# Kernel optimization log

Hardware: AMD Instinct MI355X
Metric: run time of the kernel (lower is better)

The kernel has to match this reference:

```python
import jax, jax.numpy as jnp
from jax import lax
import numpy as np

BATCH, SEQ_LEN, ENC_IN, C_OUT = 16, 512, 32, 32
N_ORDER = 256           # window_size
MULTISCALE = (1, 2, 4)
MODES = min(32, SEQ_LEN // 2)  # = 32


def make_hippo(N, dt):
    """HiPPO-LegT transition, bilinear (Tustin) discretization, Legendre eval matrix."""
    Q = np.arange(N, dtype=np.float64)
    R = (2 * Q + 1)[:, None]
    j, i = np.meshgrid(Q, Q)
    A = np.where(i < j, -1.0, (-1.0) ** (i - j + 1)) * R
    B = (-1.0) ** Q[:, None] * R                      # [N,1]
    I = np.eye(N)
    M = I - (dt / 2.0) * A
    Ad = np.linalg.solve(M, I + (dt / 2.0) * A)
    Bd = np.linalg.solve(M, dt * B).squeeze(-1)       # [N]
    vals = np.arange(0.0, 1.0, dt)
    x = 1.0 - 2.0 * vals
    P = np.zeros((N, len(vals)))
    P[0] = 1.0
    if N > 1:
        P[1] = x
    for n in range(1, N - 1):
        P[n + 1] = ((2 * n + 1) * x * P[n] - n * P[n - 1]) / (n + 1)
    E = P.T                                           # [len(vals), N]
    return Ad.astype(np.float32), Bd.astype(np.float32), E.astype(np.float32)


def setup_inputs():
    key = jax.random.key(0)
    ks = jax.random.split(key, 12)
    inp = {}
    inp['x_enc'] = jax.random.normal(ks[0], (BATCH, SEQ_LEN, ENC_IN), jnp.float32)
    inp['x_mark_enc'] = jax.random.normal(ks[1], (BATCH, SEQ_LEN, 4), jnp.float32)
    inp['x_dec'] = jax.random.normal(ks[2], (BATCH, SEQ_LEN, ENC_IN), jnp.float32)
    inp['x_mark_dec'] = jax.random.normal(ks[3], (BATCH, SEQ_LEN, 4), jnp.float32)
    inp['affine_weight'] = jnp.ones((1, 1, ENC_IN), jnp.float32)
    inp['affine_bias'] = jnp.zeros((1, 1, ENC_IN), jnp.float32)
    scale = 1.0 / (N_ORDER * N_ORDER)
    for s in range(3):
        inp[f'wr{s}'] = scale * jax.random.uniform(ks[4 + 2 * s], (N_ORDER, N_ORDER, MODES), jnp.float32)
        inp[f'wi{s}'] = scale * jax.random.uniform(ks[5 + 2 * s], (N_ORDER, N_ORDER, MODES), jnp.float32)
    inp['mlp_w'] = 0.1 * jax.random.normal(ks[10], (1, 3), jnp.float32)
    inp['mlp_b'] = jnp.zeros((1,), jnp.float32)
    inp['proj_w'] = 0.02 * jax.random.normal(ks[11], (ENC_IN, C_OUT), jnp.float32)
    inp['proj_b'] = jnp.zeros((C_OUT,), jnp.float32)
    for s, m in enumerate(MULTISCALE):
        A, Bv, E = make_hippo(N_ORDER, 1.0 / SEQ_LEN / m)
        inp[f'A{s}'] = jnp.asarray(A)
        inp[f'Bv{s}'] = jnp.asarray(Bv)
        inp[f'E{s}'] = jnp.asarray(E)
    return inp


def _hippo_scan(x, A, Bv):
    # x: [B, L, C] -> cs: [L, B, C, N]; c_t = A c_{t-1} + B f_t (applied on last dim)
    B_, L, C = x.shape
    c0 = jnp.zeros((B_, C, A.shape[0]), x.dtype)
    At = A.T
    def step(c, f):                      # f: [B, C]
        c = c @ At + f[..., None] * Bv
        return c, c
    _, cs = lax.scan(step, c0, jnp.transpose(x, (1, 0, 2)))
    return cs


def _spectral_conv(xc, wr, wi):
    # xc: [B, C, N, L]; keep first MODES rfft bins, complex channel mix over N, irfft
    L = xc.shape[-1]
    xf = jnp.fft.rfft(xc)                                # [B,C,N,L//2+1] complex64
    W = (wr + 1j * wi).astype(jnp.complex64)             # [N,N,MODES]
    out = jnp.einsum('bjix,iox->bjox', xf[..., :MODES], W)
    out_ft = jnp.pad(out, ((0, 0), (0, 0), (0, 0), (0, L // 2 + 1 - MODES)))
    return jnp.fft.irfft(out_ft, n=L)                    # [B,C,N,L]


def _forward(x_enc, affine_weight, affine_bias, specs, mlp_w, mlp_b, proj_w, proj_b, hippos):
    means = lax.stop_gradient(jnp.mean(x_enc, axis=1, keepdims=True))
    xc = x_enc - means
    stdev = lax.stop_gradient(jnp.sqrt(jnp.var(xc, axis=1, keepdims=True) + 1e-5))
    x = xc / stdev
    x = x * affine_weight + affine_bias                  # [B, L, C]
    pred_len = SEQ_LEN
    decs = []
    for (wr, wi), (A, Bv, E) in zip(specs, hippos):
        # multiscale slice x[:, -m*pred_len:] clips to full seq_len since pred_len==seq_len
        cs = _hippo_scan(x, A, Bv)                       # [L,B,C,N]
        x_in_c = jnp.transpose(cs, (1, 2, 3, 0))         # [B,C,N,L]
        out1 = _spectral_conv(x_in_c, wr, wi)            # [B,C,N,L]
        x_dec_c = out1[..., pred_len - 1]                # [B,C,N]
        dec = x_dec_c @ E[-pred_len:, :].T               # [B,C,pred_len]
        decs.append(dec)
    stacked = jnp.stack(decs, axis=-1)                   # [B,C,P,3]
    y = stacked @ mlp_w[0] + mlp_b[0]                    # Linear(3,1) + squeeze -> [B,C,P]
    y = jnp.transpose(y, (0, 2, 1))                      # [B,P,C]
    y = (y - affine_bias) / (affine_weight + 1e-10)
    y = y * stdev + means
    return y @ proj_w + proj_b                           # OutputBlock: per-step channel projection


def reference(x_enc, x_mark_enc, x_dec, x_mark_dec, affine_weight, affine_bias,
              wr0, wi0, wr1, wi1, wr2, wi2, mlp_w, mlp_b, proj_w, proj_b,
              A0, Bv0, E0, A1, Bv1, E1, A2, Bv2, E2):
    specs = [(wr0, wi0), (wr1, wi1), (wr2, wi2)]
    hippos = [(A0, Bv0, E0), (A1, Bv1, E1), (A2, Bv2, E2)]
    return _forward(x_enc, affine_weight, affine_bias, specs, mlp_w, mlp_b, proj_w, proj_b, hippos)
```

## Files before the change

### kernel.cpp

```cpp
#include <hip/hip_runtime.h>
#include <math.h>

#define SEQ 512
#define NORD 256
#define MODES 32
#define KBIG (NORD*MODES*2)
#define PI_F 3.14159265358979323846f

typedef _Float16 half8 __attribute__((ext_vector_type(8)));
typedef float floatx4 __attribute__((ext_vector_type(4)));


struct GJob {
  const float* A; const float* B; float* C; const float* scale_ptr;
  int M, N, lda, k0, k1, atomic;
};
struct GJobs { GJob j[6]; };

__global__ __launch_bounds__(256) void gemm32_k(GJobs P) {
  GJob jb = P.j[blockIdx.z];
  int col0 = blockIdx.x * 32;
  int row0 = blockIdx.y * 32;
  if (row0 >= jb.M || col0 >= jb.N) return;
  __shared__ float As[64][34];
  __shared__ float Bs[64][36];
  int tid = threadIdx.x;
  int tx = tid & 15, ty = tid >> 4;
  const float* A = jb.A; const float* B = jb.B;
  int M = jb.M, N = jb.N, lda = jb.lda;
  int kcA = (tid & 15) * 4, rA = tid >> 4;
  int ccB = (tid & 7) * 4, kkB = tid >> 3;
  int gr0 = row0 + rA, gr1 = row0 + rA + 16;
  const float4 z4 = make_float4(0.f, 0.f, 0.f, 0.f);
  float4 a0, a1, b0, b1;
  {
    int kb = jb.k0;
    a0 = (gr0 < M) ? *(const float4*)&A[(size_t)gr0 * lda + kb + kcA] : z4;
    a1 = (gr1 < M) ? *(const float4*)&A[(size_t)gr1 * lda + kb + kcA] : z4;
    b0 = *(const float4*)&B[(size_t)(kb + kkB) * N + col0 + ccB];
    b1 = *(const float4*)&B[(size_t)(kb + kkB + 32) * N + col0 + ccB];
  }
  float acc00 = 0.f, acc01 = 0.f, acc10 = 0.f, acc11 = 0.f;
  for (int kb = jb.k0; kb < jb.k1; kb += 64) {
    As[kcA+0][rA] = a0.x; As[kcA+1][rA] = a0.y; As[kcA+2][rA] = a0.z; As[kcA+3][rA] = a0.w;
    As[kcA+0][rA+16] = a1.x; As[kcA+1][rA+16] = a1.y; As[kcA+2][rA+16] = a1.z; As[kcA+3][rA+16] = a1.w;
    *(float4*)&Bs[kkB][ccB] = b0;
    *(float4*)&Bs[kkB+32][ccB] = b1;
    __syncthreads();
    if (kb + 64 < jb.k1) {
      int kn = kb + 64;
      a0 = (gr0 < M) ? *(const float4*)&A[(size_t)gr0 * lda + kn + kcA] : z4;
      a1 = (gr1 < M) ? *(const float4*)&A[(size_t)gr1 * lda + kn + kcA] : z4;
      b0 = *(const float4*)&B[(size_t)(kn + kkB) * N + col0 + ccB];
      b1 = *(const float4*)&B[(size_t)(kn + kkB + 32) * N + col0 + ccB];
    }
    #pragma unroll
    for (int k = 0; k < 64; k++) {
      float2 av = *(float2*)&As[k][ty * 2];
      float2 bv = *(float2*)&Bs[k][tx * 2];
      acc00 += av.x * bv.x; acc01 += av.x * bv.y;
      acc10 += av.y * bv.x; acc11 += av.y * bv.y;
    }
    __syncthreads();
  }
  float sc = jb.scale_ptr ? *jb.scale_ptr : 1.f;
  int gr = row0 + ty * 2, gc = col0 + tx * 2;
  float v00 = acc00 * sc, v01 = acc01 * sc, v10 = acc10 * sc, v11 = acc11 * sc;
  if (jb.atomic) {
    if (gr < M)     { atomicAdd(&jb.C[(size_t)gr * N + gc], v00);     atomicAdd(&jb.C[(size_t)gr * N + gc + 1], v01); }
    if (gr + 1 < M) { atomicAdd(&jb.C[(size_t)(gr+1) * N + gc], v10); atomicAdd(&jb.C[(size_t)(gr+1) * N + gc + 1], v11); }
  } else {
    if (gr < M)     { jb.C[(size_t)gr * N + gc] = v00;     jb.C[(size_t)gr * N + gc + 1] = v01; }
    if (gr + 1 < M) { jb.C[(size_t)(gr+1) * N + gc] = v10; jb.C[(size_t)(gr+1) * N + gc + 1] = v11; }
  }
}


__global__ __launch_bounds__(256) void prep2_k(const float* __restrict__ x_enc,
                                               const float* __restrict__ aw,
                                               const float* __restrict__ ab,
                                               float* __restrict__ F,
                                               float* __restrict__ stats,
                                               const float* A0, const float* A1, const float* A2,
                                               const float* B0, const float* B1, const float* B2,
                                               const float* E0, const float* E1, const float* E2,
                                               float* R, float* Kry, float* Et, float* Z) {
  __shared__ float tile[32][33];
  __shared__ float ws1[4], ws2[4];
  __shared__ float mean_s, istd_s;
  int bid = blockIdx.x;
  int tid = threadIdx.x;
  if (bid < 512) {
    int row = bid;
    int b = row >> 5, c = row & 31;
    const float* xp = x_enc + (size_t)b * SEQ * 32 + c;
    float v0 = xp[(size_t)tid * 32];
    float v1 = xp[(size_t)(tid + 256) * 32];
    float s = v0 + v1, s2 = v0 * v0 + v1 * v1;
    for (int off = 32; off; off >>= 1) {
      s  += __shfl_down(s,  off, 64);
      s2 += __shfl_down(s2, off, 64);
    }
    int wid = tid >> 6, lane = tid & 63;
    if (lane == 0) { ws1[wid] = s; ws2[wid] = s2; }
    __syncthreads();
    if (tid == 0) {
      float t1 = ws1[0] + ws1[1] + ws1[2] + ws1[3];
      float t2 = ws2[0] + ws2[1] + ws2[2] + ws2[3];
      float mean = t1 / 512.f;
      float var = t2 / 512.f - mean * mean;
      float sd = sqrtf(var + 1e-5f);
      mean_s = mean; istd_s = 1.f / sd;
      stats[row] = mean; stats[512 + row] = sd;
    }
    __syncthreads();
    float w = aw[c], bb = ab[c];
    float m = mean_s, is = istd_s;
    F[(size_t)row * SEQ + tid]       = (v0 - m) * is * w + bb;
    F[(size_t)row * SEQ + tid + 256] = (v1 - m) * is * w + bb;
  } else if (bid < 704) {
    int b2 = bid - 512;
    int scl = b2 >> 6, t = b2 & 63;
    int ti = t >> 3, tm = t & 7;
    const float* A = scl == 0 ? A0 : (scl == 1 ? A1 : A2);
    float* Rd = R + (size_t)scl * 2 * 65536;
    int tx = tid & 31, ty0 = tid >> 5;
    int i0 = ti * 32, m0 = tm * 32;
    #pragma unroll
    for (int r = 0; r < 4; r++) {
      int ty = ty0 + r * 8;
      tile[ty][tx] = A[(size_t)(i0 + ty) * 256 + m0 + tx];
    }
    __syncthreads();
    #pragma unroll
    for (int r = 0; r < 4; r++) {
      int ty = ty0 + r * 8;
      Rd[(size_t)(m0 + ty) * 256 + i0 + tx] = tile[tx][ty];
    }
  } else if (bid < 1088) {
    int b2 = bid - 704;
    int scl = b2 >> 7, t = b2 & 127;
    int tp = t >> 3, to = t & 7;
    const float* E; int rows;
    if (scl == 0) { E = E0; rows = 512; }
    else if (scl == 1) { E = E1; rows = 1024; }
    else { E = E2; rows = 2048; }
    int base = rows - 512;
    int p0 = tp * 32, o0 = to * 32;
    int tx = tid & 31, ty0 = tid >> 5;
    #pragma unroll
    for (int r = 0; r < 4; r++) {
      int ty = ty0 + r * 8;
      tile[ty][tx] = E[(size_t)(base + p0 + ty) * 256 + o0 + tx];
    }
    __syncthreads();
    #pragma unroll
    for (int r = 0; r < 4; r++) {
      int ty = ty0 + r * 8;
      Et[(size_t)scl * 131072 + (size_t)(o0 + ty) * 512 + p0 + tx] = tile[tx][ty];
    }
  } else if (bid < 1091) {
    int scl = bid - 1088;
    const float* B = scl == 0 ? B0 : (scl == 1 ? B1 : B2);
    Kry[(size_t)scl * 512 * 256 + tid] = B[tid];
  } else {
    int idx = (bid - 1091) * 256 + tid;
    ((float4*)Z)[idx] = make_float4(0.f, 0.f, 0.f, 0.f);
  }
}


__global__ __launch_bounds__(256) void qbuildB_k(const float* __restrict__ Kry,
                                                 const float2* __restrict__ Pp,
                                                 _Float16* __restrict__ Qf, int s0) {
  int bg = blockIdx.x;
  int slab = bg >> 8;
  int s = s0 + slab;
  int r = bg & 255;
  int ig = r & 31, c = r >> 5;
  const float* Kry_s = Kry + (size_t)s * 131072;
  const float2* P = Pp + (size_t)s * 65536;
  uint4* Qd4 = (uint4*)(Qf + (size_t)slab * 8388608);
  int tid = threadIdx.x;
  int k = tid & 31, il = tid >> 5;
  int i = ig * 8 + il;
  __shared__ __align__(16) unsigned int buf[16 * 260];
  float ar = 0.f, ai = 0.f;
  for (int cp = 0; cp < c; cp++) {
    float2 p = P[(size_t)(cp * 32 + k) * 256 + i];
    ar += p.x; ai += p.y;
  }
  const float step = 2.f * PI_F / 512.f;
  int m0 = c * 64;
  int st_low = tid & 15;
  int part_base = tid >> 4;
  for (int mb = 0; mb < 64; mb += 16) {
    #pragma unroll
    for (int mm = 0; mm < 16; mm++) {
      int m = m0 + mb + mm;
      float kap = Kry_s[(size_t)m * 256 + i];
      float sn, cn; __sincosf(step * (float)((k * m) & 511), &sn, &cn);
      ar += kap * cn; ai -= kap * sn;
      int st = 511 - m;
      float sn2, cn2; __sincosf(step * (float)((k * st) & 511), &sn2, &cn2);
      float qr = ar * cn2 + ai * sn2;
      float qi = ai * cn2 - ar * sn2;
      qr = fminf(fmaxf(qr, -60000.f), 60000.f);
      qi = fminf(fmaxf(qi, -60000.f), 60000.f);
      _Float16 h0 = (_Float16)qr, h1 = (_Float16)qi;
      unsigned short u0, u1;
      __builtin_memcpy(&u0, &h0, 2); __builtin_memcpy(&u1, &h1, 2);
      buf[(st & 15) * 260 + il * 32 + k] = (unsigned int)u0 | ((unsigned int)u1 << 16);
    }
    __syncthreads();
    int st_base = 496 - m0 - mb;
    int st = st_base + st_low;
    size_t rowbase = (size_t)(st >> 4) * 512;
    #pragma unroll
    for (int p = 0; p < 4; p++) {
      int part = part_base + p * 16;
      int ilw = part >> 3, k4 = part & 7;
      int iw = ig * 8 + ilw;
      size_t g = (rowbase + (size_t)(iw * 2 + (k4 >> 2))) * 64
               + (size_t)((k4 & 3) * 16 + st_low);
      Qd4[g] = *(const uint4*)&buf[st_low * 260 + ilw * 32 + k4 * 4];
    }
    __syncthreads();
  }
}


__global__ __launch_bounds__(256) void qw_k(const float* __restrict__ Kry,
                                            float2* __restrict__ Pp,
                                            const float* wr0, const float* wi0,
                                            const float* wr1, const float* wi1,
                                            const float* wr2, const float* wi2,
                                            _Float16* __restrict__ Wt, int s0, int nA) {
  int bid = blockIdx.x;
  int tid = threadIdx.x;
  if (bid < nA) {
    int bg = bid;
    int s = s0 + (bg >> 8);
    int r = bg & 255;
    int k = r & 31, c = r >> 5;
    const float* Kry_s = Kry + (size_t)s * 131072;
    float2* P = Pp + (size_t)s * 65536;
    int i = tid;
    float ar = 0.f, ai = 0.f;
    const float step = 2.f * PI_F / 512.f;
    int m0 = c * 64;
    for (int mm = 0; mm < 64; mm++) {
      int m = m0 + mm;
      float kap = Kry_s[(size_t)m * 256 + i];
      float sn, cn; __sincosf(step * (float)((k * m) & 511), &sn, &cn);
      ar += kap * cn; ai -= kap * sn;
    }
    P[(size_t)(c * 32 + k) * 256 + i] = make_float2(ar, ai);
  } else {
    int bg = bid - nA;
    int slab = bg >> 8;
    int s = s0 + slab;
    int r = bg & 255;
    int og = r >> 3, iq = r & 7;
    const float* wr = s == 0 ? wr0 : (s == 1 ? wr1 : wr2);
    const float* wi = s == 0 ? wi0 : (s == 1 ? wi1 : wi2);
    unsigned int* Wd = (unsigned int*)(Wt + (size_t)slab * 4194304);
    int ol = tid >> 5, k = tid & 31;
    int o = og * 8 + ol;
    float sn, cn; __sincosf((2.f * PI_F / 512.f) * (float)k, &sn, &cn);
    float g = ((k == 0) ? (1.f / 512.f) : (2.f / 512.f)) * 4096.f;
    float gc = g * cn, gs = g * sn;
    size_t obase = (size_t)(o >> 4) * 512;
    int osub = (((k >> 2) & 3) * 16 + (o & 15)) * 4 + (k & 3);
    for (int ii = 0; ii < 32; ii++) {
      int i = iq * 32 + ii;
      float a = wr[(size_t)i * 8192 + o * 32 + k];
      float b = wi[(size_t)i * 8192 + o * 32 + k];
      float v0 = gc * a + gs * b;
      float v1 = gs * a - gc * b;
      _Float16 h0 = (_Float16)v0, h1 = (_Float16)v1;
      unsigned short u0, u1;
      __builtin_memcpy(&u0, &h0, 2); __builtin_memcpy(&u1, &h1, 2);
      Wd[(obase + (size_t)(i * 2 + (k >> 4))) * 256 + osub] = (unsigned int)u0 | ((unsigned int)u1 << 16);
    }
  }
}


__global__ __launch_bounds__(256) void umfma_k(const _Float16* __restrict__ Qf,
                                               const _Float16* __restrict__ Wt,
                                               float* __restrict__ U, int s0) {
  __shared__ __align__(16) _Float16 lds[2][12288];
  int kslab = blockIdx.x;
  int y = blockIdx.y;
  int slab = blockIdx.z;
  int s = s0 + slab;
  int mtb = y >> 1, ntb = y & 1;
  const _Float16* Q = Qf + (size_t)slab * 8388608;
  const _Float16* W = Wt + (size_t)slab * 4194304;
  float* Us = U + (size_t)s * 131072;
  int tid = threadIdx.x;
  int w = tid >> 6, lane = tid & 63;
  int wm = w >> 1, wn = w & 1;
  int quad = lane >> 4, lm = lane & 15;
  int mt0g = mtb * 4;
  int nt0g = ntb * 8;
  int ktg0 = kslab * 32;
  size_t laneoff = (size_t)lane * 8;

  floatx4 acc[2][4];
  #pragma unroll
  for (int a = 0; a < 2; a++)
    #pragma unroll
    for (int b = 0; b < 4; b++) acc[a][b] = (floatx4)(0.f);

  auto stage = [&](int ks, int bufi) {
    int ktg = ktg0 + ks * 2;
    #pragma unroll
    for (int q = 0; q < 6; q++) {
      int f = w * 6 + q;
      const _Float16* src;
      if (f < 8) {
        src = Q + (((size_t)(mt0g + (f >> 1)) * 512) + (size_t)(ktg + (f & 1))) * 512;
      } else {
        int g = f - 8;
        src = W + (((size_t)(nt0g + (g >> 1)) * 512) + (size_t)(ktg + (g & 1))) * 512;
      }
      __builtin_amdgcn_global_load_lds(
          (const __attribute__((address_space(1))) unsigned int*)(src + laneoff),
          (__attribute__((address_space(3))) unsigned int*)&lds[bufi][f * 512],
          16, 0, 0);
    }
  };

  stage(0, 0);
  __syncthreads();
  int buf = 0;
  for (int ks = 0; ks < 16; ks++) {
    if (ks < 15) stage(ks + 1, buf ^ 1);
    half8 a[2][2], b[4][2];
    #pragma unroll
    for (int mi2 = 0; mi2 < 2; mi2++)
      #pragma unroll
      for (int kk = 0; kk < 2; kk++)
        a[mi2][kk] = *(const half8*)&lds[buf][(size_t)(((wm * 2 + mi2) * 2 + kk) * 512) + laneoff];
    #pragma unroll
    for (int ni2 = 0; ni2 < 4; ni2++)
      #pragma unroll
      for (int kk = 0; kk < 2; kk++)
        b[ni2][kk] = *(const half8*)&lds[buf][(size_t)(4096 + ((wn * 4 + ni2) * 2 + kk) * 512) + laneoff];
    #pragma unroll
    for (int kk = 0; kk < 2; kk++)
      #pragma unroll
      for (int mi2 = 0; mi2 < 2; mi2++)
        #pragma unroll
        for (int ni2 = 0; ni2 < 4; ni2++)
          acc[mi2][ni2] = __builtin_amdgcn_mfma_f32_16x16x32_f16(a[mi2][kk], b[ni2][kk], acc[mi2][ni2], 0, 0, 0);
    __syncthreads();
    buf ^= 1;
  }

  const float sc = 1.f / 4096.f;
  #pragma unroll
  for (int mi2 = 0; mi2 < 2; mi2++) {
    int R0 = (mt0g + wm * 2 + mi2) * 16 + quad * 4;
    #pragma unroll
    for (int ni2 = 0; ni2 < 4; ni2++) {
      int gc = (nt0g + wn * 4 + ni2) * 16 + lm;
      #pragma unroll
      for (int rr2 = 0; rr2 < 4; rr2++)
        atomicAdd(&Us[(size_t)(R0 + rr2) * 256 + gc], acc[mi2][ni2][rr2] * sc);
    }
  }
}


__global__ __launch_bounds__(256) void final_k(const float* __restrict__ y0,
                                               const float* __restrict__ stats,
                                               const float* __restrict__ aw,
                                               const float* __restrict__ ab,
                                               const float* __restrict__ mlp_b,
                                               const float* __restrict__ pw,
                                               const float* __restrict__ pb,
                                               float* __restrict__ out) {
  int b = blockIdx.y;
  int p0 = blockIdx.x * 8;
  int tid = threadIdx.x;
  __shared__ float ys[32 * 8];
  __shared__ float pws[32 * 32];
  for (int t = tid; t < 1024; t += 256) pws[t] = pw[t];
  int c = tid >> 3, pl = tid & 7;
  int row = b * 32 + c;
  float mean = stats[row], sd = stats[512 + row];
  float raw = y0[(size_t)row * 512 + p0 + pl];
  float v = ((raw + mlp_b[0]) - ab[c]) / (aw[c] + 1e-10f) * sd + mean;
  ys[c * 8 + pl] = v;
  __syncthreads();
  int co = tid & 31; int pl2 = tid >> 5;
  float accv = pb[co];
  #pragma unroll
  for (int cc = 0; cc < 32; cc++) accv += ys[cc * 8 + pl2] * pws[cc * 32 + co];
  out[(size_t)b * 512 * 32 + (size_t)(p0 + pl2) * 32 + co] = accv;
}


extern "C" void kernel_launch(void* const* d_in, const int* in_sizes, int n_in,
                              void* d_out, int out_size, void* d_ws, size_t ws_size,
                              hipStream_t stream) {
  const float* x_enc = (const float*)d_in[0];
  const float* aw = (const float*)d_in[4];
  const float* ab = (const float*)d_in[5];
  const float* wr[3] = {(const float*)d_in[6], (const float*)d_in[8], (const float*)d_in[10]};
  const float* wi[3] = {(const float*)d_in[7], (const float*)d_in[9], (const float*)d_in[11]};
  const float* mlp_w = (const float*)d_in[12];
  const float* mlp_b = (const float*)d_in[13];
  const float* proj_w = (const float*)d_in[14];
  const float* proj_b = (const float*)d_in[15];
  const float* Am[3]  = {(const float*)d_in[16], (const float*)d_in[19], (const float*)d_in[22]};
  const float* Bv[3]  = {(const float*)d_in[17], (const float*)d_in[20], (const float*)d_in[23]};
  const float* Em[3]  = {(const float*)d_in[18], (const float*)d_in[21], (const float*)d_in[24]};

  float* w = (float*)d_ws;
  float* F     = w; w += 512 * 512;
  float* stats = w; w += 1024;
  float* Kry   = w; w += 3 * 512 * 256;
  float* R     = w; w += 3 * 2 * 65536;
  float* U     = w; w += 3 * 512 * 256;
  float* Ttot  = w; w += 512 * 512;
  float* Et    = w; w += 3 * 256 * 512;
  float* y0    = w; w += 512 * 512;
  float* Pp    = w; w += 3 * 65536 * 2;
  _Float16* Qf = (_Float16*)w;

  size_t base_bytes = (size_t)((char*)Qf - (char*)d_ws);
  size_t slab_bytes = (size_t)(8388608 + 4194304) * 2;
  int nS = (ws_size >= base_bytes + 3 * slab_bytes) ? 3 : 1;
  _Float16* Wb = Qf + (size_t)nS * 8388608;

  prep2_k<<<1731, 256, 0, stream>>>(x_enc, aw, ab, F, stats,
                                    Am[0], Am[1], Am[2], Bv[0], Bv[1], Bv[2],
                                    Em[0], Em[1], Em[2], R, Kry, Et, U);

  for (int j = 0; j < 9; j++) {
    GJobs P{};
    int M = 1 << j;
    int cur = j & 1;
    int nz = 0;
    for (int s = 0; s < 3; s++) {
      float* Ks = Kry + (size_t)s * 131072;
      float* Rj = R + (size_t)s * 131072 + (size_t)cur * 65536;
      float* Rn = R + (size_t)s * 131072 + (size_t)(1 - cur) * 65536;
      P.j[nz++] = {Ks, Rj, Ks + (size_t)M * 256, nullptr, M, 256, 256, 0, 256, 0};
      if (j < 8) P.j[nz++] = {Rj, Rj, Rn, nullptr, 256, 256, 256, 0, 256, 0};
    }
    gemm32_k<<<dim3(8, 8, nz), 256, 0, stream>>>(P);
  }

  if (nS == 3) {
    qw_k<<<1536, 256, 0, stream>>>(Kry, (float2*)Pp, wr[0], wi[0], wr[1], wi[1],
                                   wr[2], wi[2], Wb, 0, 768);
    qbuildB_k<<<768, 256, 0, stream>>>(Kry, (const float2*)Pp, Qf, 0);
    umfma_k<<<dim3(16, 16, 3), 256, 0, stream>>>(Qf, Wb, U, 0);
  } else {
    for (int s = 0; s < 3; s++) {
      qw_k<<<512, 256, 0, stream>>>(Kry, (float2*)Pp, wr[0], wi[0], wr[1], wi[1],
                                    wr[2], wi[2], Wb, s, 256);
      qbuildB_k<<<256, 256, 0, stream>>>(Kry, (const float2*)Pp, Qf, s);
      umfma_k<<<dim3(16, 16, 1), 256, 0, stream>>>(Qf, Wb, U, s);
    }
  }

  {
    GJobs P{};
    for (int s = 0; s < 3; s++)
      P.j[s] = {U + (size_t)s * 131072, Et + (size_t)s * 131072, Ttot,
                mlp_w + s, 512, 512, 256, 0, 256, 1};
    gemm32_k<<<dim3(16, 16, 3), 256, 0, stream>>>(P);
  }

  {
    GJobs P{};
    P.j[0] = {F, Ttot, y0, nullptr, 512, 512, 512, 0, 512, 0};
    gemm32_k<<<dim3(16, 16, 1), 256, 0, stream>>>(P);
  }

  final_k<<<dim3(64, 16), 256, 0, stream>>>(y0, stats, aw, ab, mlp_b, proj_w, proj_b,
                                            (float*)d_out);
}
```

Before: 351.8 us.

## Fuse Krylov doubling GEMMs into cooperative kernel and move weight packing into prep

Replaces nine separate gemm32 launches for the Krylov power-doubling steps with one cooperative kernel that loops over steps, using grid-wide syncs between them and a register-prefetched tile loop. It also moves the fp16 spectral-weight packing out of qw_k into extra blocks of the prep kernel, so that work overlaps with the other prep tasks, and halves qw_k's grid. This is meant to cut launch overhead and idle gaps between the small dependent GEMMs. In exchange it relies on cooperative launch support and grid.sync cost, and falls back to the old launches if the cooperative launch fails.

```diff
diff --git a/kernel.cpp b/kernel.cpp
--- a/kernel.cpp
+++ b/kernel.cpp
@@ -1,5 +1,8 @@
 #include <hip/hip_runtime.h>
+#include <hip/hip_cooperative_groups.h>
 #include <math.h>
+
+namespace cg = cooperative_groups;
 
 #define SEQ 512
 #define NORD 256
@@ -76,6 +79,81 @@
 }
 
 
+__global__ __launch_bounds__(256) void kry_k(float* __restrict__ Kry,
+                                             float* __restrict__ R) {
+  cg::grid_group grid = cg::this_grid();
+  __shared__ float As[64][34];
+  __shared__ float Bs[64][36];
+  int tid = threadIdx.x;
+  int tx = tid & 15, ty = tid >> 4;
+  int kcA = (tid & 15) * 4, rA = tid >> 4;
+  int ccB = (tid & 7) * 4, kkB = tid >> 3;
+  const float4 z4 = make_float4(0.f, 0.f, 0.f, 0.f);
+  for (int j = 0; j < 9; j++) {
+    int M = 1 << j;
+    int mb = (M + 31) >> 5;
+    int tilesA = mb * 8;
+    int hasB = (j < 8) ? 64 : 0;
+    int tilesPer = tilesA + hasB;
+    int ntiles = tilesPer * 3;
+    int cur = j & 1;
+    for (int t = blockIdx.x; t < ntiles; t += gridDim.x) {
+      int s = t / tilesPer;
+      int r = t - s * tilesPer;
+      float* Ks = Kry + (size_t)s * 131072;
+      float* Rj = R + (size_t)s * 131072 + (size_t)cur * 65536;
+      float* Rn = R + (size_t)s * 131072 + (size_t)(1 - cur) * 65536;
+      const float* A; const float* B; float* C;
+      int Mj, row0, col0;
+      if (r < tilesA) {
+        A = Ks; B = Rj; C = Ks + (size_t)M * 256; Mj = M;
+        row0 = (r >> 3) * 32; col0 = (r & 7) * 32;
+      } else {
+        int r2 = r - tilesA;
+        A = Rj; B = Rj; C = Rn; Mj = 256;
+        row0 = (r2 >> 3) * 32; col0 = (r2 & 7) * 32;
+      }
+      int gr0 = row0 + rA, gr1 = row0 + rA + 16;
+      float4 a0, a1, b0, b1;
+      a0 = (gr0 < Mj) ? *(const float4*)&A[(size_t)gr0 * 256 + kcA] : z4;
+      a1 = (gr1 < Mj) ? *(const float4*)&A[(size_t)gr1 * 256 + kcA] : z4;
+      b0 = *(const float4*)&B[(size_t)kkB * 256 + col0 + ccB];
+      b1 = *(const float4*)&B[(size_t)(kkB + 32) * 256 + col0 + ccB];
+      float acc00 = 0.f, acc01 = 0.f, acc10 = 0.f, acc11 = 0.f;
+      for (int kb = 0; kb < 256; kb += 64) {
+        As[kcA+0][rA] = a0.x; As[kcA+1][rA] = a0.y; As[kcA+2][rA] = a0.z; As[kcA+3][rA] = a0.w;
+        As[kcA+0][rA+16] = a1.x; As[kcA+1][rA+16] = a1.y; As[kcA+2][rA+16] = a1.z; As[kcA+3][rA+16] = a1.w;
+        *(float4*)&Bs[kkB][ccB] = b0;
+        *(float4*)&Bs[kkB+32][ccB] = b1;
+        __syncthreads();
+        if (kb + 64 < 256) {
+          int kn = kb + 64;
+          a0 = (gr0 < Mj) ? *(const float4*)&A[(size_t)gr0 * 256 + kn + kcA] : z4;
+          a1 = (gr1 < Mj) ? *(const float4*)&A[(size_t)gr1 * 256 + kn + kcA] : z4;
+          b0 = *(const float4*)&B[(size_t)(kn + kkB) * 256 + col0 + ccB];
+          b1 = *(const float4*)&B[(size_t)(kn + kkB + 32) * 256 + col0 + ccB];
+        }
+        #pragma unroll
+        for (int k = 0; k < 64; k++) {
+          float2 av = *(float2*)&As[k][ty * 2];
+          float2 bv = *(float2*)&Bs[k][tx * 2];
+          acc00 += av.x * bv.x; acc01 += av.x * bv.y;
+          acc10 += av.y * bv.x; acc11 += av.y * bv.y;
+        }
+        __syncthreads();
+      }
+      int gr = row0 + ty * 2, gc = col0 + tx * 2;
+      if (gr < Mj)     { C[(size_t)gr * 256 + gc] = acc00;     C[(size_t)gr * 256 + gc + 1] = acc01; }
+      if (gr + 1 < Mj) { C[(size_t)(gr+1) * 256 + gc] = acc10; C[(size_t)(gr+1) * 256 + gc + 1] = acc11; }
+    }
+    if (j < 8) {
+      __threadfence();
+      grid.sync();
+    }
+  }
+}
+
+
 __global__ __launch_bounds__(256) void prep2_k(const float* __restrict__ x_enc,
                                                const float* __restrict__ aw,
                                                const float* __restrict__ ab,
@@ -84,7 +162,11 @@
                                                const float* A0, const float* A1, const float* A2,
                                                const float* B0, const float* B1, const float* B2,
                                                const float* E0, const float* E1, const float* E2,
-                                               float* R, float* Kry, float* Et, float* Z) {
+                                               float* R, float* Kry, float* Et, float* Z,
+                                               const float* wr0, const float* wi0,
+                                               const float* wr1, const float* wi1,
+                                               const float* wr2, const float* wi2,
+                                               _Float16* __restrict__ Wt) {
   __shared__ float tile[32][33];
   __shared__ float ws1[4], ws2[4];
   __shared__ float mean_s, istd_s;
@@ -163,9 +245,36 @@
     int scl = bid - 1088;
     const float* B = scl == 0 ? B0 : (scl == 1 ? B1 : B2);
     Kry[(size_t)scl * 512 * 256 + tid] = B[tid];
-  } else {
+  } else if (bid < 1731) {
     int idx = (bid - 1091) * 256 + tid;
     ((float4*)Z)[idx] = make_float4(0.f, 0.f, 0.f, 0.f);
+  } else {
+    int bg = bid - 1731;
+    int slab = bg >> 8;
+    int s = slab;
+    int r = bg & 255;
+    int og = r >> 3, iq = r & 7;
+    const float* wr = s == 0 ? wr0 : (s == 1 ? wr1 : wr2);
+    const float* wi = s == 0 ? wi0 : (s == 1 ? wi1 : wi2);
+    unsigned int* Wd = (unsigned int*)(Wt + (size_t)slab * 4194304);
+    int ol = tid >> 5, k = tid & 31;
+    int o = og * 8 + ol;
+    float sn, cn; __sincosf((2.f * PI_F / 512.f) * (float)k, &sn, &cn);
+    float g = ((k == 0) ? (1.f / 512.f) : (2.f / 512.f)) * 4096.f;
+    float gc = g * cn, gs = g * sn;
+    size_t obase = (size_t)(o >> 4) * 512;
+    int osub = (((k >> 2) & 3) * 16 + (o & 15)) * 4 + (k & 3);
+    for (int ii = 0; ii < 32; ii++) {
+      int i = iq * 32 + ii;
+      float a = wr[(size_t)i * 8192 + o * 32 + k];
+      float b = wi[(size_t)i * 8192 + o * 32 + k];
+      float v0 = gc * a + gs * b;
+      float v1 = gs * a - gc * b;
+      _Float16 h0 = (_Float16)v0, h1 = (_Float16)v1;
+      unsigned short u0, u1;
+      __builtin_memcpy(&u0, &h0, 2); __builtin_memcpy(&u1, &h1, 2);
+      Wd[(obase + (size_t)(i * 2 + (k >> 4))) * 256 + osub] = (unsigned int)u0 | ((unsigned int)u1 << 16);
+    }
   }
 }
 
@@ -437,28 +546,37 @@
   int nS = (ws_size >= base_bytes + 3 * slab_bytes) ? 3 : 1;
   _Float16* Wb = Qf + (size_t)nS * 8388608;
 
-  prep2_k<<<1731, 256, 0, stream>>>(x_enc, aw, ab, F, stats,
-                                    Am[0], Am[1], Am[2], Bv[0], Bv[1], Bv[2],
-                                    Em[0], Em[1], Em[2], R, Kry, Et, U);
-
-  for (int j = 0; j < 9; j++) {
-    GJobs P{};
-    int M = 1 << j;
-    int cur = j & 1;
-    int nz = 0;
-    for (int s = 0; s < 3; s++) {
-      float* Ks = Kry + (size_t)s * 131072;
-      float* Rj = R + (size_t)s * 131072 + (size_t)cur * 65536;
-      float* Rn = R + (size_t)s * 131072 + (size_t)(1 - cur) * 65536;
-      P.j[nz++] = {Ks, Rj, Ks + (size_t)M * 256, nullptr, M, 256, 256, 0, 256, 0};
-      if (j < 8) P.j[nz++] = {Rj, Rj, Rn, nullptr, 256, 256, 256, 0, 256, 0};
-    }
-    gemm32_k<<<dim3(8, 8, nz), 256, 0, stream>>>(P);
+  int nW = (nS == 3) ? 768 : 0;
+  prep2_k<<<1731 + nW, 256, 0, stream>>>(x_enc, aw, ab, F, stats,
+                                         Am[0], Am[1], Am[2], Bv[0], Bv[1], Bv[2],
+                                         Em[0], Em[1], Em[2], R, Kry, Et, U,
+                                         wr[0], wi[0], wr[1], wi[1], wr[2], wi[2], Wb);
+
+  {
+    void* args[] = { (void*)&Kry, (void*)&R };
+    hipError_t ce = hipLaunchCooperativeKernel((void*)kry_k, dim3(512), dim3(256),
+                                               args, 0, stream);
+    if (ce != hipSuccess) {
+      for (int j = 0; j < 9; j++) {
+        GJobs P{};
+        int M = 1 << j;
+        int cur = j & 1;
+        int nz = 0;
+        for (int s = 0; s < 3; s++) {
+          float* Ks = Kry + (size_t)s * 131072;
+          float* Rj = R + (size_t)s * 131072 + (size_t)cur * 65536;
+          float* Rn = R + (size_t)s * 131072 + (size_t)(1 - cur) * 65536;
+          P.j[nz++] = {Ks, Rj, Ks + (size_t)M * 256, nullptr, M, 256, 256, 0, 256, 0};
+          if (j < 8) P.j[nz++] = {Rj, Rj, Rn, nullptr, 256, 256, 256, 0, 256, 0};
+        }
+        gemm32_k<<<dim3(8, 8, nz), 256, 0, stream>>>(P);
+      }
+    }
   }
 
   if (nS == 3) {
-    qw_k<<<1536, 256, 0, stream>>>(Kry, (float2*)Pp, wr[0], wi[0], wr[1], wi[1],
-                                   wr[2], wi[2], Wb, 0, 768);
+    qw_k<<<768, 256, 0, stream>>>(Kry, (float2*)Pp, wr[0], wi[0], wr[1], wi[1],
+                                  wr[2], wi[2], Wb, 0, 768);
     qbuildB_k<<<768, 256, 0, stream>>>(Kry, (const float2*)Pp, Qf, 0);
     umfma_k<<<dim3(16, 16, 3), 256, 0, stream>>>(Qf, Wb, U, 0);
   } else {
```

Result: slower. 1.142 ms (+224.7%).
